# Performance work log

Hardware: AMD Instinct MI355X
Metric: run time of the kernel (lower is better)

Reference implementation:

```python
import jax, jax.numpy as jnp
import numpy as np

NEG_INF = -1000.0
EPS = 1e-5

M, B, D = 1024, 8, 1024
H = 16
DH = D // H
FF = 4096


def _layer_norm(x, g, b):
    mu = jnp.mean(x, axis=-1, keepdims=True)
    var = jnp.mean((x - mu) ** 2, axis=-1, keepdims=True)
    return (x - mu) * jax.lax.rsqrt(var + EPS) * g + b


def setup_inputs() -> dict:
    key = jax.random.key(0)
    ks = jax.random.split(key, 12)
    s = 0.02
    return {
        "x": jax.random.normal(ks[0], (M, B, D), jnp.float32),
        "src_mask": jnp.zeros((M, B), jnp.bool_),
        "ln1_g": jnp.ones((D,), jnp.float32),
        "ln1_b": jnp.zeros((D,), jnp.float32),
        "wq": jax.random.normal(ks[1], (D, D), jnp.float32) * s,
        "bq": jnp.zeros((D,), jnp.float32),
        "wk": jax.random.normal(ks[2], (D, D), jnp.float32) * s,
        "bk": jnp.zeros((D,), jnp.float32),
        "wv": jax.random.normal(ks[3], (D, D), jnp.float32) * s,
        "bv": jnp.zeros((D,), jnp.float32),
        "wo": jax.random.normal(ks[4], (D, D), jnp.float32) * s,
        "bo": jnp.zeros((D,), jnp.float32),
        "ln2_g": jnp.ones((D,), jnp.float32),
        "ln2_b": jnp.zeros((D,), jnp.float32),
        "w1": jax.random.normal(ks[5], (D, FF), jnp.float32) * s,
        "b1": jnp.zeros((FF,), jnp.float32),
        "w2": jax.random.normal(ks[6], (FF, D), jnp.float32) * s,
        "b2": jnp.zeros((D,), jnp.float32),
    }


def reference(x, src_mask, ln1_g, ln1_b, wq, bq, wk, bk, wv, bv, wo, bo,
              ln2_g, ln2_b, w1, b1, w2, b2):
    m, bsz, d = x.shape
    # --- self-attention sublayer ---
    xn = _layer_norm(x, ln1_g, ln1_b)
    q = (xn @ wq + bq).reshape(m, bsz, H, DH)
    k = (xn @ wk + bk).reshape(m, bsz, H, DH)
    v = (xn @ wv + bv).reshape(m, bsz, H, DH)
    # NOTE: original has NO 1/sqrt(head_dim) scaling
    potentials = jnp.einsum('mbhi,nbhj->mnbh', q, k)  # [m,n,b,h]
    potentials = jnp.where(src_mask[None, :, :, None], NEG_INF, potentials)
    weights = jax.nn.softmax(potentials, axis=1)
    pooled = jnp.einsum('mnbh,nbhi->mbhi', weights, v).reshape(m, bsz, d)
    att = pooled @ wo + bo
    x = x + att
    # --- feed-forward sublayer ---
    xn = _layer_norm(x, ln2_g, ln2_b)
    h = jax.nn.relu(xn @ w1 + b1)
    return h @ w2 + b2 + x
```

## Files before the change

kernel.cpp:

```cpp
#include <hip/hip_runtime.h>
#include <hip/hip_bf16.h>

typedef float fv4 __attribute__((ext_vector_type(4)));
typedef __bf16 bfv8 __attribute__((ext_vector_type(8)));
typedef unsigned short u16;

#define DEV static __device__ __forceinline__

DEV u16 f2bf(float f) {
  union { __hip_bfloat16 h; u16 u; } c;
  c.h = __float2bfloat16(f);
  return c.u;
}

DEV void glds16(const void* g, void* l) {
  __builtin_amdgcn_global_load_lds(
      (const __attribute__((address_space(1))) unsigned int*)g,
      (__attribute__((address_space(3))) unsigned int*)l, 16, 0, 0);
}

DEV fv4 mfma16(bfv8 a, bfv8 b, fv4 c) {
  return __builtin_amdgcn_mfma_f32_16x16x32_bf16(a, b, c, 0, 0, 0);
}

template <bool OUT_BF16, bool RELU, bool RESID, bool BIAS>
__global__ __launch_bounds__(256, 2) void gemm_k(
    const u16* __restrict__ A, const u16* __restrict__ Bt,
    const float* __restrict__ bias, const float* __restrict__ resid,
    void* __restrict__ outp, int K, int N, int lda, int ldb) {
  __shared__ __align__(16) u16 lds[2][2][128 * 32];
  const int tid = threadIdx.x;
  const int lane = tid & 63, wid = tid >> 6;
  const int gx = gridDim.x;
  const int nwg = gx * gridDim.y;
  int wg = blockIdx.y * gx + blockIdx.x;
  wg = (wg & 7) * (nwg >> 3) + (wg >> 3);
  const int bm0 = (wg / gx) * 128, bn0 = (wg % gx) * 128;
  const int wr = (wid >> 1) * 64, wc = (wid & 1) * 64;
  const int g = lane >> 4, ml = lane & 15;

  fv4 acc[4][4];
#pragma unroll
  for (int i = 0; i < 4; ++i)
#pragma unroll
    for (int j = 0; j < 4; ++j) acc[i][j] = (fv4)0.f;

  const int nK = K >> 5;

  auto stage = [&](int t) {
    const int buf = t & 1;
    const int k0 = t * 32;
#pragma unroll
    for (int p = 0; p < 2; ++p) {
      const int s = p * 256 + tid;
      const int r0 = ((s >> 2) & 1) ^ ((s >> 4) & 1);
      const int row = ((s >> 3) << 1) | r0;
      const int chunk = (s & 3) ^ (row & 3);
      glds16(A + (size_t)(bm0 + row) * lda + k0 + chunk * 8,
             &lds[buf][0][(p * 256 + wid * 64) * 8]);
      glds16(Bt + (size_t)(bn0 + row) * ldb + k0 + chunk * 8,
             &lds[buf][1][(p * 256 + wid * 64) * 8]);
    }
  };

  stage(0);
  for (int t = 0; t < nK; ++t) {
    __syncthreads();
    if (t + 1 < nK) stage(t + 1);
    const u16* Ab = lds[t & 1][0];
    const u16* Bb = lds[t & 1][1];
    bfv8 af[4], bf[4];
#pragma unroll
    for (int f = 0; f < 4; ++f) {
      const int ra = wr + f * 16 + ml;
      const int ba = ((ra << 6) + (g << 4)) ^ ((ra & 7) << 4);
      af[f] = *(const bfv8*)&Ab[ba >> 1];
      const int rb = wc + f * 16 + ml;
      const int bb = ((rb << 6) + (g << 4)) ^ ((rb & 7) << 4);
      bf[f] = *(const bfv8*)&Bb[bb >> 1];
    }
#pragma unroll
    for (int i = 0; i < 4; ++i)
#pragma unroll
      for (int j = 0; j < 4; ++j) acc[i][j] = mfma16(af[i], bf[j], acc[i][j]);
  }

#pragma unroll
  for (int j = 0; j < 4; ++j) {
    const int n = bn0 + wc + j * 16 + ml;
    float bv = 0.f;
    if (BIAS) bv = bias[n];
#pragma unroll
    for (int i = 0; i < 4; ++i) {
      const int m0r = bm0 + wr + i * 16 + g * 4;
#pragma unroll
      for (int r = 0; r < 4; ++r) {
        float val = acc[i][j][r] + bv;
        if (RESID) val += resid[(size_t)(m0r + r) * N + n];
        if (RELU) val = fmaxf(val, 0.f);
        if (OUT_BF16)
          ((u16*)outp)[(size_t)(m0r + r) * N + n] = f2bf(val);
        else
          ((float*)outp)[(size_t)(m0r + r) * N + n] = val;
      }
    }
  }
}

__global__ __launch_bounds__(256) void vt_k(const u16* __restrict__ v,
                                            u16* __restrict__ vt) {
  __shared__ __align__(16) u16 Tl[64 * 72];
  const int bh = blockIdx.y, b = bh >> 4, h = bh & 15;
  const int nt = blockIdx.x;
  const int t = threadIdx.x;

#pragma unroll
  for (int p = 0; p < 2; ++p) {
    const int cidx = p * 256 + t;
    const int j = cidx >> 3, c = cidx & 7;
    bfv8 val = *(const bfv8*)&v[((size_t)(nt * 64 + j) * 8 + b) * 1024 +
                                h * 64 + c * 8];
    *(bfv8*)&Tl[j * 72 + c * 8] = val;
  }
  __syncthreads();

#pragma unroll
  for (int p = 0; p < 2; ++p) {
    const int cidx = p * 256 + t;
    const int dh = cidx >> 3, nc = cidx & 7;
    u16 tmp[8];
#pragma unroll
    for (int jj = 0; jj < 8; ++jj) tmp[jj] = Tl[(nc * 8 + jj) * 72 + dh];
    *(bfv8*)&vt[((size_t)(bh * 64 + dh)) * 1024 + nt * 64 +
                (nc ^ (dh & 7)) * 8] = *(const bfv8*)tmp;
  }
}

__global__ __launch_bounds__(256, 2) void attn3_k(
    const u16* __restrict__ vt, const float* __restrict__ qsarr,
    const float* __restrict__ ksarr, const unsigned char* __restrict__ mask,
    u16* __restrict__ pooled) {
  __shared__ float ks_s[1024];
  __shared__ float red[16];
  __shared__ int anym_s;
  __shared__ float zl[4][4][16];
  __shared__ __align__(16) u16 VT[2][64 * 64];
  __shared__ __align__(16) u16 stg[4][16 * 72];

  const int tid = threadIdx.x, lane = tid & 63, wid = tid >> 6;
  const int g = lane >> 4, ml = lane & 15;
  const int bh = blockIdx.y, b = bh >> 4, h = bh & 15;
  const int mbase = blockIdx.x * 256 + wid * 64;

  if (tid == 0) anym_s = 0;
  __syncthreads();

  const float* ksp = ksarr + (size_t)bh * 1024;
  float4 kv = *(const float4*)&ksp[tid * 4];
  *(float4*)&ks_s[tid * 4] = kv;
  const float kvv[4] = {kv.x, kv.y, kv.z, kv.w};
  float mx = -3.4e38f, mn = 3.4e38f;
  int am = 0;
#pragma unroll
  for (int j = 0; j < 4; ++j) {
    const int n = tid * 4 + j;
    const int mk = mask[(size_t)n * 8 + b] ? 1 : 0;
    am |= mk;
    if (!mk) { mx = fmaxf(mx, kvv[j]); mn = fminf(mn, kvv[j]); }
  }
  if (am) atomicOr(&anym_s, 1);
#pragma unroll
  for (int s = 1; s <= 32; s <<= 1) {
    mx = fmaxf(mx, __shfl_xor(mx, s, 64));
    mn = fminf(mn, __shfl_xor(mn, s, 64));
  }
  if (lane == 0) { red[wid] = mx; red[8 + wid] = mn; }
  __syncthreads();
  const float smax = fmaxf(fmaxf(red[0], red[1]), fmaxf(red[2], red[3]));
  const float smin = fminf(fminf(red[8], red[9]), fminf(red[10], red[11]));
  const int anym = anym_s;

  float c[4], M[4];
#pragma unroll
  for (int mf = 0; mf < 4; ++mf) {
    c[mf] = qsarr[(size_t)bh * 1024 + mbase + mf * 16 + ml];
    M[mf] = (c[mf] >= 0.f) ? c[mf] * smax : c[mf] * smin;
  }

  fv4 o[4][4];
#pragma unroll
  for (int mf = 0; mf < 4; ++mf)
#pragma unroll
    for (int d = 0; d < 4; ++d) o[mf][d] = (fv4)0.f;
  float zacc[4] = {0.f, 0.f, 0.f, 0.f};

  const size_t vtbase = (size_t)bh * 64 * 1024;
  auto stageV = [&](int nt) {
    const int buf = nt & 1;
#pragma unroll
    for (int p = 0; p < 2; ++p) {
      const int s = p * 256 + tid;
      glds16(&vt[vtbase + (size_t)(s >> 3) * 1024 + nt * 64 + (s & 7) * 8],
             &VT[buf][s * 8]);
    }
  };

  stageV(0);
  for (int nt = 0; nt < 16; ++nt) {
    __syncthreads();
    if (nt + 1 < 16) stageV(nt + 1);
    const u16* Vb = VT[nt & 1];
    const int n0 = nt * 64;
#pragma unroll
    for (int kk = 0; kk < 2; ++kk) {
      const int kb = n0 + kk * 32 + g * 8;
      const float4 s0 = *(const float4*)&ks_s[kb];
      const float4 s1 = *(const float4*)&ks_s[kb + 4];
      const float sv[8] = {s0.x, s0.y, s0.z, s0.w, s1.x, s1.y, s1.z, s1.w};
      int mk[8] = {0, 0, 0, 0, 0, 0, 0, 0};
      if (anym) {
#pragma unroll
        for (int j = 0; j < 8; ++j) mk[j] = mask[(size_t)(kb + j) * 8 + b];
      }
      bfv8 pa[4];
#pragma unroll
      for (int mf = 0; mf < 4; ++mf) {
        u16 tmp[8];
#pragma unroll
        for (int j = 0; j < 8; ++j) {
          float p = __expf(fmaf(c[mf], sv[j], -M[mf]));
          if (anym && mk[j]) p = 0.f;
          zacc[mf] += p;
          tmp[j] = f2bf(p);
        }
        pa[mf] = *(const bfv8*)tmp;
      }
#pragma unroll
      for (int ds = 0; ds < 4; ++ds) {
        const int d = ds * 16 + ml;
        const int pc = (kk * 4 + g) ^ (d & 7);
        bfv8 vf = *(const bfv8*)&Vb[d * 64 + pc * 8];
#pragma unroll
        for (int mf = 0; mf < 4; ++mf)
          o[mf][ds] = mfma16(pa[mf], vf, o[mf][ds]);
      }
    }
  }

#pragma unroll
  for (int mf = 0; mf < 4; ++mf) {
    zacc[mf] += __shfl_xor(zacc[mf], 16, 64);
    zacc[mf] += __shfl_xor(zacc[mf], 32, 64);
  }
  if (g == 0) {
#pragma unroll
    for (int mf = 0; mf < 4; ++mf) zl[wid][mf][ml] = zacc[mf];
  }
  asm volatile("" ::: "memory");

#pragma unroll
  for (int mf = 0; mf < 4; ++mf) {
    float zin[4];
#pragma unroll
    for (int r = 0; r < 4; ++r) zin[r] = 1.f / zl[wid][mf][g * 4 + r];
#pragma unroll
    for (int ds = 0; ds < 4; ++ds)
#pragma unroll
      for (int r = 0; r < 4; ++r)
        stg[wid][(g * 4 + r) * 72 + ds * 16 + ml] =
            f2bf(o[mf][ds][r] * zin[r]);
    asm volatile("" ::: "memory");
#pragma unroll
    for (int p = 0; p < 2; ++p) {
      const int ch = p * 64 + lane;
      const int mr = ch >> 3, cc = ch & 7;
      bfv8 val = *(const bfv8*)&stg[wid][mr * 72 + cc * 8];
      *(bfv8*)&pooled[((size_t)(mbase + mf * 16 + mr) * 8 + b) * 1024 +
                      h * 64 + cc * 8] = val;
    }
    asm volatile("" ::: "memory");
  }
}

__global__ __launch_bounds__(256) void ln_k(
    const float* __restrict__ x, const float* __restrict__ gw,
    const float* __restrict__ bw, u16* __restrict__ out) {
  __shared__ float sm[8];
  const int row = blockIdx.x, tid = threadIdx.x;
  const int lane = tid & 63, wid = tid >> 6;
  const float4 xv = *(const float4*)&x[(size_t)row * 1024 + tid * 4];
  float s = xv.x + xv.y + xv.z + xv.w;
  float q = xv.x * xv.x + xv.y * xv.y + xv.z * xv.z + xv.w * xv.w;
#pragma unroll
  for (int m = 1; m <= 32; m <<= 1) {
    s += __shfl_xor(s, m, 64);
    q += __shfl_xor(q, m, 64);
  }
  if (lane == 0) { sm[wid] = s; sm[4 + wid] = q; }
  __syncthreads();
  s = sm[0] + sm[1] + sm[2] + sm[3];
  q = sm[4] + sm[5] + sm[6] + sm[7];
  const float mean = s * (1.f / 1024.f);
  const float var = q * (1.f / 1024.f) - mean * mean;
  const float rstd = rsqrtf(var + 1e-5f);
  const float4 gv = *(const float4*)&gw[tid * 4];
  const float4 bv = *(const float4*)&bw[tid * 4];
  ushort4 ov;
  ov.x = f2bf((xv.x - mean) * rstd * gv.x + bv.x);
  ov.y = f2bf((xv.y - mean) * rstd * gv.y + bv.y);
  ov.z = f2bf((xv.z - mean) * rstd * gv.z + bv.z);
  ov.w = f2bf((xv.w - mean) * rstd * gv.w + bv.w);
  *(ushort4*)&out[(size_t)row * 1024 + tid * 4] = ov;
}

__global__ __launch_bounds__(256) void qks2_k(
    const float* __restrict__ x, const float* __restrict__ A,
    const float* __restrict__ S12, float* __restrict__ qsarr,
    float* __restrict__ ksarr) {
  __shared__ __align__(16) float Alds[128 * 36];
  __shared__ float wred[4][8][2][32];
  __shared__ float wred2[4][8][2][2];
  __shared__ float rowstat[16][2];

  const int t = threadIdx.x;
  const int rowp = t & 7, sub = t >> 3;
  const int wid = t >> 6, lane = t & 63;
  const int r0 = blockIdx.x * 16;

  float acc[2][32];
#pragma unroll
  for (int rr = 0; rr < 2; ++rr)
#pragma unroll
    for (int i = 0; i < 32; ++i) acc[rr][i] = 0.f;
  float sx[2] = {0.f, 0.f}, sq[2] = {0.f, 0.f};

  for (int ch = 0; ch < 8; ++ch) {
    __syncthreads();
#pragma unroll
    for (int j = 0; j < 4; ++j) {
      const int f = t + 256 * j;
      const float4 av = *(const float4*)&A[ch * 4096 + f * 4];
      *(float4*)&Alds[(f >> 3) * 36 + (f & 7) * 4] = av;
    }
    __syncthreads();
#pragma unroll
    for (int rr = 0; rr < 2; ++rr) {
      const int row = r0 + rowp * 2 + rr;
      const float4 xv = *(const float4*)&x[(size_t)row * 1024 + ch * 128 + sub * 4];
      const float xs[4] = {xv.x, xv.y, xv.z, xv.w};
#pragma unroll
      for (int kk = 0; kk < 4; ++kk) {
        sx[rr] += xs[kk];
        sq[rr] = fmaf(xs[kk], xs[kk], sq[rr]);
        const float* ap = &Alds[(sub * 4 + kk) * 36];
#pragma unroll
        for (int i = 0; i < 32; ++i)
          acc[rr][i] = fmaf(xs[kk], ap[i], acc[rr][i]);
      }
    }
  }

#pragma unroll
  for (int m = 8; m <= 32; m <<= 1) {
#pragma unroll
    for (int rr = 0; rr < 2; ++rr) {
      sx[rr] += __shfl_xor(sx[rr], m, 64);
      sq[rr] += __shfl_xor(sq[rr], m, 64);
#pragma unroll
      for (int i = 0; i < 32; ++i)
        acc[rr][i] += __shfl_xor(acc[rr][i], m, 64);
    }
  }
  if (lane < 8) {
#pragma unroll
    for (int rr = 0; rr < 2; ++rr) {
#pragma unroll
      for (int i = 0; i < 32; ++i) wred[wid][lane][rr][i] = acc[rr][i];
      wred2[wid][lane][rr][0] = sx[rr];
      wred2[wid][lane][rr][1] = sq[rr];
    }
  }
  __syncthreads();

  if (t < 16) {
    float s = 0.f, q = 0.f;
#pragma unroll
    for (int w = 0; w < 4; ++w) {
      s += wred2[w][t >> 1][t & 1][0];
      q += wred2[w][t >> 1][t & 1][1];
    }
    const float mu = s * (1.f / 1024.f);
    const float var = q * (1.f / 1024.f) - mu * mu;
    rowstat[t][0] = mu;
    rowstat[t][1] = rsqrtf(var + 1e-5f);
  }
  __syncthreads();

#pragma unroll
  for (int o = 0; o < 2; ++o) {
    const int idx = t * 2 + o;
    const int rl = idx >> 5, h = idx & 31;
    const float dot = wred[0][rl >> 1][rl & 1][h] + wred[1][rl >> 1][rl & 1][h] +
                      wred[2][rl >> 1][rl & 1][h] + wred[3][rl >> 1][rl & 1][h];
    const float mu = rowstat[rl][0], rstd = rowstat[rl][1];
    const float val = rstd * (dot - mu * S12[h]) + S12[32 + h];
    const int row = r0 + rl, mm = row >> 3, bb = row & 7;
    if (h < 16)
      qsarr[(size_t)(bb * 16 + h) * 1024 + mm] = val;
    else
      ksarr[(size_t)(bb * 16 + h - 16) * 1024 + mm] = val;
  }
}

__global__ void wsum_k(const float* __restrict__ wq,
                       const float* __restrict__ wk,
                       float* __restrict__ wqsa) {
  const int k = blockIdx.x, t = threadIdx.x;
  const int h32 = t >> 3, ch = t & 7;
  const float* src = (h32 < 16) ? (wq + (size_t)k * 1024 + h32 * 64 + ch * 8)
                                : (wk + (size_t)k * 1024 + (h32 - 16) * 64 + ch * 8);
  float s = 0.f;
#pragma unroll
  for (int j = 0; j < 8; ++j) s += src[j];
  s += __shfl_xor(s, 1, 64);
  s += __shfl_xor(s, 2, 64);
  s += __shfl_xor(s, 4, 64);
  if (ch == 0) wqsa[k * 32 + h32] = s;
}

__global__ void bsum_k(const float* __restrict__ bq,
                       const float* __restrict__ bk,
                       float* __restrict__ bqks) {
  const int t = threadIdx.x;
  if (t < 32) {
    const float* s = (t < 16) ? (bq + t * 64) : (bk + (t - 16) * 64);
    float a = 0.f;
    for (int j = 0; j < 64; ++j) a += s[j];
    bqks[t] = a;
  }
}

__global__ void afill_k(const float* __restrict__ wqsa,
                        const float* __restrict__ g,
                        float* __restrict__ A) {
  const int f = blockIdx.x * 256 + threadIdx.x;
  const float gv = g[f >> 3];
  const float4 wv = *(const float4*)&wqsa[f * 4];
  float4 av;
  av.x = wv.x * gv; av.y = wv.y * gv; av.z = wv.z * gv; av.w = wv.w * gv;
  *(float4*)&A[f * 4] = av;
}

__global__ void s12_k(const float* __restrict__ wqsa,
                      const float* __restrict__ g,
                      const float* __restrict__ lb,
                      const float* __restrict__ bqks,
                      float* __restrict__ S12) {
  __shared__ float red1[8][32], red2[8][32];
  const int t = threadIdx.x;
  const int h = t & 31, seg = t >> 5;
  float s1 = 0.f, s2 = 0.f;
  for (int k = seg * 128; k < seg * 128 + 128; ++k) {
    const float a = wqsa[k * 32 + h];
    s1 = fmaf(g[k], a, s1);
    s2 = fmaf(lb[k], a, s2);
  }
  red1[seg][h] = s1;
  red2[seg][h] = s2;
  __syncthreads();
  if (t < 32) {
    float a1 = 0.f, a2 = 0.f;
#pragma unroll
    for (int s = 0; s < 8; ++s) { a1 += red1[s][t]; a2 += red2[s][t]; }
    S12[t] = a1;
    S12[32 + t] = a2 + bqks[t];
  }
}

__global__ void tr_k(const float* __restrict__ W, u16* __restrict__ Wt,
                     int R, int C) {
  __shared__ float tile[32][33];
  const int x = threadIdx.x, y = threadIdx.y;
  const int c0 = blockIdx.x * 32, r0 = blockIdx.y * 32;
#pragma unroll
  for (int i = 0; i < 4; ++i)
    tile[y + i * 8][x] = W[(size_t)(r0 + y + i * 8) * C + c0 + x];
  __syncthreads();
#pragma unroll
  for (int i = 0; i < 4; ++i)
    Wt[(size_t)(c0 + y + i * 8) * R + r0 + x] = f2bf(tile[x][y + i * 8]);
}

extern "C" void kernel_launch(void* const* d_in, const int* in_sizes, int n_in,
                              void* d_out, int out_size, void* d_ws,
                              size_t ws_size, hipStream_t stream) {
  const float* x = (const float*)d_in[0];
  const unsigned char* mask = (const unsigned char*)d_in[1];
  const float* ln1g = (const float*)d_in[2];
  const float* ln1b = (const float*)d_in[3];
  const float* wq = (const float*)d_in[4];
  const float* bq = (const float*)d_in[5];
  const float* wk = (const float*)d_in[6];
  const float* bk = (const float*)d_in[7];
  const float* wv = (const float*)d_in[8];
  const float* bv = (const float*)d_in[9];
  const float* wo = (const float*)d_in[10];
  const float* bo = (const float*)d_in[11];
  const float* ln2g = (const float*)d_in[12];
  const float* ln2b = (const float*)d_in[13];
  const float* w1 = (const float*)d_in[14];
  const float* b1 = (const float*)d_in[15];
  const float* w2 = (const float*)d_in[16];
  const float* b2 = (const float*)d_in[17];

  u16* wvT = (u16*)d_ws;
  u16* woT = wvT + 1024 * 1024;
  u16* w1T = woT + 1024 * 1024;
  u16* w2T = w1T + 4096 * 1024;
  float* wqsa = (float*)(w2T + 1024 * 4096);
  float* bqks = wqsa + 1024 * 32;
  float* Aq = bqks + 32;
  float* S12 = Aq + 1024 * 32;
  float* qsarr = S12 + 64;
  float* ksarr = qsarr + 8 * 16 * 1024;
  u16* v = (u16*)(ksarr + 8 * 16 * 1024);
  u16* pooled = v + (size_t)8192 * 1024;
  u16* xn = pooled + (size_t)8192 * 1024;
  u16* vtb = xn + (size_t)8192 * 1024;
  u16* hbuf = v;
  float* x2 = (float*)d_out;

  const dim3 b256(256), btr(32, 8);
  tr_k<<<dim3(32, 32), btr, 0, stream>>>(wv, wvT, 1024, 1024);
  tr_k<<<dim3(32, 32), btr, 0, stream>>>(wo, woT, 1024, 1024);
  tr_k<<<dim3(128, 32), btr, 0, stream>>>(w1, w1T, 1024, 4096);
  tr_k<<<dim3(32, 128), btr, 0, stream>>>(w2, w2T, 4096, 1024);
  wsum_k<<<dim3(1024), b256, 0, stream>>>(wq, wk, wqsa);
  bsum_k<<<dim3(1), dim3(64), 0, stream>>>(bq, bk, bqks);
  afill_k<<<dim3(32), b256, 0, stream>>>(wqsa, ln1g, Aq);
  s12_k<<<dim3(1), b256, 0, stream>>>(wqsa, ln1g, ln1b, bqks, S12);

  ln_k<<<dim3(8192), b256, 0, stream>>>(x, ln1g, ln1b, xn);
  qks2_k<<<dim3(512), b256, 0, stream>>>(x, Aq, S12, qsarr, ksarr);
  gemm_k<true, false, false, true><<<dim3(8, 64), b256, 0, stream>>>(
      xn, wvT, bv, nullptr, v, 1024, 1024, 1024, 1024);
  vt_k<<<dim3(16, 128), b256, 0, stream>>>(v, vtb);
  attn3_k<<<dim3(4, 128), b256, 0, stream>>>(vtb, qsarr, ksarr, mask, pooled);
  gemm_k<false, false, true, true><<<dim3(8, 64), b256, 0, stream>>>(
      pooled, woT, bo, x, x2, 1024, 1024, 1024, 1024);
  ln_k<<<dim3(8192), b256, 0, stream>>>(x2, ln2g, ln2b, xn);
  gemm_k<true, true, false, true><<<dim3(16, 64), b256, 0, stream>>>(
      xn, w1T, b1, nullptr, hbuf, 1024, 2048, 1024, 1024);
  gemm_k<false, false, true, true><<<dim3(8, 64), b256, 0, stream>>>(
      hbuf, w2T, b2, x2, x2, 2048, 1024, 2048, 4096);
  gemm_k<true, true, false, true><<<dim3(16, 64), b256, 0, stream>>>(
      xn, w1T + (size_t)2048 * 1024, b1 + 2048, nullptr, hbuf, 1024, 2048,
      1024, 1024);
  gemm_k<false, false, true, false><<<dim3(8, 64), b256, 0, stream>>>(
      hbuf, w2T + 2048, nullptr, x2, x2, 2048, 1024, 2048, 4096);
}
```

Measured before the change: 477.1 us.

## Add 256x256-tile double-buffered GEMM kernel for FFN up-projection

Introduces gemm256_k, a 512-thread kernel that computes 256x256 output tiles with double-buffered LDS staging via global_load_lds, an XOR-swizzled layout, and s_setprio around the MFMA bursts. It replaces the 128x128 gemm_k for the two FFN first-layer GEMMs (xn @ w1 halves, with ReLU and bf16 output). Larger tiles raise arithmetic intensity and cut global and LDS traffic per FLOP. The cost is higher register and LDS pressure and fewer blocks (256 per launch), which may underfill the CUs.

```diff
diff --git a/kernel.cpp b/kernel.cpp
--- a/kernel.cpp
+++ b/kernel.cpp
@@ -96,6 +96,106 @@
 #pragma unroll
       for (int r = 0; r < 4; ++r) {
         float val = acc[i][j][r] + bv;
+        if (RESID) val += resid[(size_t)(m0r + r) * N + n];
+        if (RELU) val = fmaxf(val, 0.f);
+        if (OUT_BF16)
+          ((u16*)outp)[(size_t)(m0r + r) * N + n] = f2bf(val);
+        else
+          ((float*)outp)[(size_t)(m0r + r) * N + n] = val;
+      }
+    }
+  }
+}
+
+template <bool OUT_BF16, bool RELU, bool RESID, bool BIAS>
+__global__ __launch_bounds__(512, 2) void gemm256_k(
+    const u16* __restrict__ A, const u16* __restrict__ Bt,
+    const float* __restrict__ bias, const float* __restrict__ resid,
+    void* __restrict__ outp, int K, int N, int lda, int ldb) {
+  __shared__ __align__(16) u16 Abuf[2][256 * 32];
+  __shared__ __align__(16) u16 Bbuf[2][256 * 32];
+  const int tid = threadIdx.x;
+  const int lane = tid & 63, wid = tid >> 6;
+  const int bm0 = blockIdx.y * 256, bn0 = blockIdx.x * 256;
+  const int wr = wid >> 2, wc = wid & 3;
+  const int g = lane >> 4, ml = lane & 15;
+
+  fv4 acc[8][4];
+#pragma unroll
+  for (int i = 0; i < 8; ++i)
+#pragma unroll
+    for (int j = 0; j < 4; ++j) acc[i][j] = (fv4)0.f;
+
+  const int nT = K >> 5;
+
+  auto stage = [&](int t) {
+    const int buf = t & 1;
+    const int k0 = t * 32;
+#pragma unroll
+    for (int p = 0; p < 2; ++p) {
+      const int s = p * 512 + tid;
+      const int r0 = ((s >> 2) & 1) ^ ((s >> 4) & 1);
+      const int row = ((s >> 3) << 1) | r0;
+      const int chunk = (s & 3) ^ (row & 3);
+      glds16(A + (size_t)(bm0 + row) * lda + k0 + chunk * 8,
+             &Abuf[buf][(p * 512 + wid * 64) * 8]);
+      glds16(Bt + (size_t)(bn0 + row) * ldb + k0 + chunk * 8,
+             &Bbuf[buf][(p * 512 + wid * 64) * 8]);
+    }
+  };
+
+  stage(0);
+  for (int t = 0; t < nT; ++t) {
+    if (t + 1 < nT) {
+      stage(t + 1);
+      asm volatile("s_waitcnt vmcnt(4)" ::: "memory");
+    } else {
+      asm volatile("s_waitcnt vmcnt(0)" ::: "memory");
+    }
+    __builtin_amdgcn_s_barrier();
+    asm volatile("" ::: "memory");
+
+    const u16* Ab = Abuf[t & 1];
+    const u16* Bb = Bbuf[t & 1];
+    bfv8 bf[4];
+#pragma unroll
+    for (int nf = 0; nf < 4; ++nf) {
+      const int rb = wc * 64 + nf * 16 + ml;
+      const int bb = ((rb << 6) + (g << 4)) ^ ((rb & 7) << 4);
+      bf[nf] = *(const bfv8*)&Bb[bb >> 1];
+    }
+#pragma unroll
+    for (int mh = 0; mh < 2; ++mh) {
+      bfv8 af[4];
+#pragma unroll
+      for (int f = 0; f < 4; ++f) {
+        const int ra = wr * 128 + (mh * 4 + f) * 16 + ml;
+        const int ba = ((ra << 6) + (g << 4)) ^ ((ra & 7) << 4);
+        af[f] = *(const bfv8*)&Ab[ba >> 1];
+      }
+      __builtin_amdgcn_s_setprio(1);
+#pragma unroll
+      for (int f = 0; f < 4; ++f)
+#pragma unroll
+        for (int nf = 0; nf < 4; ++nf)
+          acc[mh * 4 + f][nf] = mfma16(af[f], bf[nf], acc[mh * 4 + f][nf]);
+      __builtin_amdgcn_s_setprio(0);
+    }
+    asm volatile("" ::: "memory");
+    __builtin_amdgcn_s_barrier();
+  }
+
+#pragma unroll
+  for (int nf = 0; nf < 4; ++nf) {
+    const int n = bn0 + wc * 64 + nf * 16 + ml;
+    float bv = 0.f;
+    if (BIAS) bv = bias[n];
+#pragma unroll
+    for (int mf = 0; mf < 8; ++mf) {
+      const int m0r = bm0 + wr * 128 + mf * 16 + g * 4;
+#pragma unroll
+      for (int r = 0; r < 4; ++r) {
+        float val = acc[mf][nf][r] + bv;
         if (RESID) val += resid[(size_t)(m0r + r) * N + n];
         if (RELU) val = fmaxf(val, 0.f);
         if (OUT_BF16)
@@ -549,11 +649,11 @@
   gemm_k<false, false, true, true><<<dim3(8, 64), b256, 0, stream>>>(
       pooled, woT, bo, x, x2, 1024, 1024, 1024, 1024);
   ln_k<<<dim3(8192), b256, 0, stream>>>(x2, ln2g, ln2b, xn);
-  gemm_k<true, true, false, true><<<dim3(16, 64), b256, 0, stream>>>(
+  gemm256_k<true, true, false, true><<<dim3(8, 32), dim3(512), 0, stream>>>(
       xn, w1T, b1, nullptr, hbuf, 1024, 2048, 1024, 1024);
   gemm_k<false, false, true, true><<<dim3(8, 64), b256, 0, stream>>>(
       hbuf, w2T, b2, x2, x2, 2048, 1024, 2048, 4096);
-  gemm_k<true, true, false, true><<<dim3(16, 64), b256, 0, stream>>>(
+  gemm256_k<true, true, false, true><<<dim3(8, 32), dim3(512), 0, stream>>>(
       xn, w1T + (size_t)2048 * 1024, b1 + 2048, nullptr, hbuf, 1024, 2048,
       1024, 1024);
   gemm_k<false, false, true, false><<<dim3(8, 64), b256, 0, stream>>>(
```

Result: slower. 503.5 us (+5.6%).
